# Optimization experiments

Measured on AMD Instinct MI355X. Metric: run time of the kernel, lower is better.

## Reference

```python
import jax, jax.numpy as jnp
import numpy as np
import math

B, T, C, H = 4, 2048, 1024, 16
D = C // H  # head dim = 64


def setup_inputs() -> dict:
    key = jax.random.key(0)
    ks = jax.random.split(key, 5)
    scale = 0.02
    x = jax.random.normal(ks[0], (B, T, C), dtype=jnp.float32)
    # torch nn.Linear(n_embd, 3*n_embd): weight [3C, C]; we store transposed [C, 3C]
    W_kqv = jax.random.normal(ks[1], (C, 3 * C), dtype=jnp.float32) * scale
    b_kqv = jnp.zeros((3 * C,), dtype=jnp.float32)
    W_proj = jax.random.normal(ks[2], (C, C), dtype=jnp.float32) * scale
    b_proj = jnp.zeros((C,), dtype=jnp.float32)
    padding_mask = jnp.ones((B, T), dtype=jnp.int32)  # 1 = valid token
    return {"x": x, "W_kqv": W_kqv, "b_kqv": b_kqv, "W_proj": W_proj,
            "b_proj": b_proj, "padding_mask": padding_mask}


def reference(x, W_kqv, b_kqv, W_proj, b_proj, padding_mask):
    Bx, Tx, Cx = x.shape
    kqv = x @ W_kqv + b_kqv                      # [B,T,3C]
    # original splits as k, q, v (in that order)
    k, q, v = jnp.split(kqv, 3, axis=2)
    def heads(t):
        return t.reshape(Bx, Tx, H, D).transpose(0, 2, 1, 3)  # [B,H,T,D]
    k, q, v = heads(k), heads(q), heads(v)
    att = jnp.einsum('bhqd,bhkd->bhqk', q, k) * (1.0 / math.sqrt(D))  # [B,H,T,T]
    causal = jnp.tril(jnp.ones((Tx, Tx), dtype=bool))[None, None]     # [1,1,T,T]
    valid = causal & (padding_mask[:, None, None, :] != 0)            # [B,1,T,T] broadcast
    neg_inf = jnp.finfo(att.dtype).min
    att = jnp.where(valid, att, neg_inf)
    att = jax.nn.softmax(att, axis=-1)
    y = jnp.einsum('bhqk,bhkd->bhqd', att, v)    # [B,H,T,D]
    y = y.transpose(0, 2, 1, 3).reshape(Bx, Tx, Cx)
    return y @ W_proj + b_proj
```

## Files before the change

### kernel.cpp

```cpp
#include <hip/hip_runtime.h>


typedef short bf16x8 __attribute__((ext_vector_type(8)));
typedef float floatx4 __attribute__((ext_vector_type(4)));

#define MFMA16(a, b, c) __builtin_amdgcn_mfma_f32_16x16x32_bf16(a, b, c, 0, 0, 0)

#define ASYNC_COPY16(gp, lp)                                                   \
  __builtin_amdgcn_global_load_lds(                                            \
      (__attribute__((address_space(1))) void*)(gp),                           \
      (__attribute__((address_space(3))) void*)(lp), 16, 0, 0)

#define DRAIN_VMCNT() asm volatile("s_waitcnt vmcnt(0)" ::: "memory")
#define WAIT_VMCNT6() asm volatile("s_waitcnt vmcnt(6)" ::: "memory")

#if defined(__has_builtin)
#if __has_builtin(__builtin_amdgcn_exp2f)
#define EXP2(x) __builtin_amdgcn_exp2f(x)
#endif
#endif
#ifndef EXP2
#define EXP2(x) exp2f(x)
#endif

__device__ __forceinline__ short f2bf(float f) {
  union { float f; unsigned u; } c;
  c.f = f;
  unsigned r = c.u + 0x7fffu + ((c.u >> 16) & 1u);
  return (short)(r >> 16);
}

__global__ __launch_bounds__(256) void prep(const float* __restrict__ x,
                                            short* __restrict__ xb,
                                            const float* __restrict__ Wkqv,
                                            short* __restrict__ Wkqvt,
                                            const float* __restrict__ Wproj,
                                            short* __restrict__ Wprojt) {
  __shared__ float buf[64][65];
  const int t = threadIdx.x;
  const int bx = blockIdx.x;
  if (bx < 8192) {
    int i = (bx * 256 + t) * 4;
    float4 v = *(const float4*)&x[i];
    short4 o;
    o.x = f2bf(v.x); o.y = f2bf(v.y); o.z = f2bf(v.z); o.w = f2bf(v.w);
    *(short4*)&xb[i] = o;
    return;
  }
  const int tb = bx - 8192;
  const int nb = tb & 63, kb = tb >> 6;
  const float* in;
  short* out;
  int N, n0;
  if (nb < 48) { in = Wkqv; out = Wkqvt; N = 3072; n0 = nb * 64; }
  else         { in = Wproj; out = Wprojt; N = 1024; n0 = (nb - 48) * 64; }
  const int k0 = kb * 64;
#pragma unroll
  for (int i = 0; i < 4; ++i) {
    int s = t + i * 256;
    int row = s >> 4, c4 = (s & 15) * 4;
    float4 v = *(const float4*)&in[(size_t)(k0 + row) * N + n0 + c4];
    buf[row][c4] = v.x; buf[row][c4 + 1] = v.y;
    buf[row][c4 + 2] = v.z; buf[row][c4 + 3] = v.w;
  }
  __syncthreads();
#pragma unroll
  for (int i = 0; i < 2; ++i) {
    int u = t + i * 256;
    int rn = u >> 3, ch = (u & 7) * 8;
    short tmp[8];
#pragma unroll
    for (int j = 0; j < 8; ++j) tmp[j] = f2bf(buf[ch + j][rn]);
    *(uint4*)&out[(size_t)(n0 + rn) * 1024 + k0 + ch] = *(uint4*)tmp;
  }
}

template <int MODE>
__global__ __launch_bounds__(512, 2) void gemm_ph256(const short* __restrict__ A,
                                                     const short* __restrict__ Bt,
                                                     const float* __restrict__ bias,
                                                     void* __restrict__ Cout,
                                                     int M, int N, int K) {
  __shared__ short smem[73728];
  const int tid = threadIdx.x;
  const int lane = tid & 63;
  const int wv = tid >> 6;
  const int l15 = lane & 15, quad = lane >> 4;
  const int xr = l15 & 7;
  int lin = blockIdx.y * gridDim.x + blockIdx.x;
  const int nwg = gridDim.x * gridDim.y;
  lin = (lin & 7) * (nwg >> 3) + (lin >> 3);
  const int bx = lin % gridDim.x, by = lin / gridDim.x;
  const int m0 = by * 128, n0 = bx * 256;
  const int wm = (wv >> 2) * 64, wn = (wv & 3) * 64;
  const int NT = K >> 6;

  floatx4 acc[4][4] = {};

#define STAGE_A(kt, bs, j)                                                     \
  { int c_ = (j) * 512 + tid;                                                  \
    int r_ = c_ >> 3, ch_ = (c_ & 7) ^ (r_ & 7);                               \
    ASYNC_COPY16(&A[(size_t)(m0 + r_) * K + (kt) * 64 + ch_ * 8],              \
                 &smem[(bs) * 8192 + c_ * 8]); }
#define STAGE_B(kt, bs, j)                                                     \
  { int c_ = (j) * 512 + tid;                                                  \
    int r_ = c_ >> 3, ch_ = (c_ & 7) ^ (r_ & 7);                               \
    ASYNC_COPY16(&Bt[(size_t)(n0 + r_) * K + (kt) * 64 + ch_ * 8],             \
                 &smem[24576 + (bs) * 16384 + c_ * 8]); }

  STAGE_A(0, 0, 0); STAGE_A(0, 0, 1);
  STAGE_B(0, 0, 0); STAGE_B(0, 0, 1); STAGE_B(0, 0, 2); STAGE_B(0, 0, 3);
  STAGE_A(1, 1, 0); STAGE_A(1, 1, 1);
  STAGE_B(1, 1, 0); STAGE_B(1, 1, 1); STAGE_B(1, 1, 2); STAGE_B(1, 1, 3);
  WAIT_VMCNT6();
  __builtin_amdgcn_s_barrier();

  int cur = 0, nxt = 2;
  for (int kt = 0; kt < NT; ++kt) {
    const bool st = (kt + 2 < NT);
    const short* Asr = &smem[cur * 8192];
    const short* Bsr = &smem[24576 + cur * 16384];

    if (st) { STAGE_A(kt + 2, nxt, 0); STAGE_A(kt + 2, nxt, 1); STAGE_B(kt + 2, nxt, 0); }
    bf16x8 af[4][2], bf0[2][2];
#pragma unroll
    for (int mi = 0; mi < 4; ++mi)
#pragma unroll
      for (int s = 0; s < 2; ++s)
        af[mi][s] = *(const bf16x8*)
            &Asr[(wm + mi * 16 + l15) * 64 + (((s * 4 + quad) ^ xr) * 8)];
#pragma unroll
    for (int nj = 0; nj < 2; ++nj)
#pragma unroll
      for (int s = 0; s < 2; ++s)
        bf0[nj][s] = *(const bf16x8*)
            &Bsr[(wn + nj * 16 + l15) * 64 + (((s * 4 + quad) ^ xr) * 8)];
    __builtin_amdgcn_s_setprio(1);
#pragma unroll
    for (int s = 0; s < 2; ++s)
#pragma unroll
      for (int mi = 0; mi < 4; ++mi)
#pragma unroll
        for (int nj = 0; nj < 2; ++nj)
          acc[mi][nj] = MFMA16(af[mi][s], bf0[nj][s], acc[mi][nj]);
    __builtin_amdgcn_s_setprio(0);
    __builtin_amdgcn_s_barrier();

    if (st) { STAGE_B(kt + 2, nxt, 1); STAGE_B(kt + 2, nxt, 2); STAGE_B(kt + 2, nxt, 3); }
    bf16x8 bf1[2][2];
#pragma unroll
    for (int nj = 0; nj < 2; ++nj)
#pragma unroll
      for (int s = 0; s < 2; ++s)
        bf1[nj][s] = *(const bf16x8*)
            &Bsr[(wn + (2 + nj) * 16 + l15) * 64 + (((s * 4 + quad) ^ xr) * 8)];
    __builtin_amdgcn_s_setprio(1);
#pragma unroll
    for (int s = 0; s < 2; ++s)
#pragma unroll
      for (int mi = 0; mi < 4; ++mi)
#pragma unroll
        for (int nj = 0; nj < 2; ++nj)
          acc[mi][2 + nj] = MFMA16(af[mi][s], bf1[nj][s], acc[mi][2 + nj]);
    __builtin_amdgcn_s_setprio(0);
    if (st) { WAIT_VMCNT6(); } else { DRAIN_VMCNT(); }
    __builtin_amdgcn_s_barrier();
    cur = (cur == 2) ? 0 : cur + 1;
    nxt = (nxt == 2) ? 0 : nxt + 1;
  }
#undef STAGE_A
#undef STAGE_B

  {
    short* outs = (short*)Cout;
    const size_t QOFF = (size_t)64 * 2048 * 64;
    const int sec = n0 >> 10;
    short* Es = smem;
    if (sec < 2) {
#pragma unroll
      for (int ni = 0; ni < 4; ++ni) {
        int c = wn + ni * 16 + l15;
        float bv = bias[n0 + c];
#pragma unroll
        for (int mi = 0; mi < 4; ++mi) {
          int r0 = wm + mi * 16 + quad * 4;
#pragma unroll
          for (int rr = 0; rr < 4; ++rr) {
            int r = r0 + rr;
            Es[r * 256 + (c ^ (((r >> 2) & 3) << 4))] = f2bf(acc[mi][ni][rr] + bv);
          }
        }
      }
    } else {
#pragma unroll
      for (int ni = 0; ni < 4; ++ni) {
        int c = wn + ni * 16 + l15;
        float bv = bias[n0 + c];
#pragma unroll
        for (int mi = 0; mi < 4; ++mi) {
          int r0 = wm + mi * 16 + quad * 4;
#pragma unroll
          for (int rr = 0; rr < 4; ++rr) {
            int r = r0 + rr;
            Es[c * 128 + (r ^ ((c & 7) << 3))] = f2bf(acc[mi][ni][rr] + bv);
          }
        }
      }
    }
    __syncthreads();
    if (sec < 2) {
#pragma unroll
      for (int jj = 0; jj < 8; ++jj) {
        int idx = jj * 512 + tid;
        int rr2 = idx >> 5;
        int cc2 = (idx & 31) * 8;
        uint4 v = *(const uint4*)&Es[rr2 * 256 + (cc2 ^ (((rr2 >> 2) & 3) << 4))];
        int colg = n0 + cc2;
        int hh = (colg >> 6) & 15, dd = colg & 63;
        int row = m0 + rr2, bb = row >> 11, tt = row & 2047;
        *(uint4*)(outs + (size_t)sec * QOFF +
                  (((size_t)(bb * 16 + hh) * 2048 + tt) * 64 + dd)) = v;
      }
    } else {
#pragma unroll
      for (int jj = 0; jj < 8; ++jj) {
        int idx = jj * 512 + tid;
        int cd = idx >> 4;
        int rb = (idx & 15) * 8;
        uint4 v = *(const uint4*)&Es[cd * 128 + (rb ^ ((cd & 7) << 3))];
        int colg = n0 + cd;
        int hh = (colg >> 6) & 15, dd = colg & 63;
        int trow = m0 + rb, bb = trow >> 11, tt = trow & 2047;
        *(uint4*)(outs + 2 * QOFF +
                  ((size_t)(bb * 16 + hh) * 64 + dd) * 2048 + tt) = v;
      }
    }
  }
}

__global__ __launch_bounds__(256, 2) void gemm_dbuf128(const short* __restrict__ A,
                                                       const short* __restrict__ Bt,
                                                       const float* __restrict__ bias,
                                                       float* __restrict__ outf,
                                                       int M, int N, int K) {
  __shared__ short As[2][8192];
  __shared__ short Bs[2][8192];
  const int tid = threadIdx.x;
  const int lane = tid & 63;
  const int wv = tid >> 6;
  const int l15 = lane & 15, quad = lane >> 4;
  const int xr = l15 & 7;
  int lin = blockIdx.y * gridDim.x + blockIdx.x;
  const int nwg = gridDim.x * gridDim.y;
  lin = (lin & 7) * (nwg >> 3) + (lin >> 3);
  const int bx = lin & (gridDim.x - 1), by = lin / gridDim.x;
  const int m0 = by * 128, n0 = bx * 128;
  const int wm = (wv >> 1) * 64, wn = (wv & 1) * 64;
  const int NT = K >> 6;

  floatx4 acc[4][4] = {};

#define STAGE_AB(kt, bs)                                                       \
  { _Pragma("unroll")                                                          \
    for (int j_ = 0; j_ < 4; ++j_) {                                           \
      int c_ = j_ * 256 + tid;                                                 \
      int r_ = c_ >> 3, ch_ = (c_ & 7) ^ (r_ & 7);                             \
      ASYNC_COPY16(&A[(size_t)(m0 + r_) * K + (kt) * 64 + ch_ * 8],            \
                   &As[bs][c_ * 8]);                                           \
      ASYNC_COPY16(&Bt[(size_t)(n0 + r_) * K + (kt) * 64 + ch_ * 8],           \
                   &Bs[bs][c_ * 8]);                                           \
    } }

  STAGE_AB(0, 0);
  DRAIN_VMCNT();
  __syncthreads();

  int cur = 0;
  for (int kt = 0; kt < NT; ++kt) {
    if (kt + 1 < NT) STAGE_AB(kt + 1, cur ^ 1);
#pragma unroll
    for (int s = 0; s < 2; ++s) {
      const int chs = ((s * 4 + quad) ^ xr) * 8;
      bf16x8 af[4], bfr[4];
#pragma unroll
      for (int i = 0; i < 4; ++i) {
        af[i]  = *(const bf16x8*)&As[cur][(wm + i * 16 + l15) * 64 + chs];
        bfr[i] = *(const bf16x8*)&Bs[cur][(wn + i * 16 + l15) * 64 + chs];
      }
#pragma unroll
      for (int mi = 0; mi < 4; ++mi)
#pragma unroll
        for (int ni = 0; ni < 4; ++ni)
          acc[mi][ni] = MFMA16(af[mi], bfr[ni], acc[mi][ni]);
    }
    DRAIN_VMCNT();
    __syncthreads();
    cur ^= 1;
  }
#undef STAGE_AB

#pragma unroll
  for (int ni = 0; ni < 4; ++ni) {
    int col = n0 + wn + ni * 16 + l15;
    float bv = bias[col];
#pragma unroll
    for (int mi = 0; mi < 4; ++mi) {
#pragma unroll
      for (int rr = 0; rr < 4; ++rr) {
        int row = m0 + wm + mi * 16 + quad * 4 + rr;
        outf[(size_t)row * N + col] = acc[mi][ni][rr] + bv;
      }
    }
  }
}

__global__ __launch_bounds__(256, 3) void attn_flash8(const short* __restrict__ Qd,
                                                      const short* __restrict__ Kd,
                                                      const short* __restrict__ Vd,
                                                      const int* __restrict__ pmask,
                                                      short* __restrict__ y) {
  constexpr int T = 2048, C = 1024;
  __shared__ short Ks[2][64 * 64];
  __shared__ short Vs[2][64 * 64];
  __shared__ short Ps[4][32][64];

  const int tid = threadIdx.x;
  const int lane = tid & 63, w = tid >> 6;
  const int l15 = lane & 15, quad = lane >> 4;
  const int xr = l15 & 7;
  const int lin = blockIdx.x;
  const int qb = 15 - (lin >> 6);
  const int bh = lin & 63;
  const int b = bh >> 4, h = bh & 15;
  const short* Qb = Qd + (size_t)bh * T * 64;
  const short* Kb = Kd + (size_t)bh * T * 64;
  const short* Vb = Vd + (size_t)bh * 64 * T;
  const int* pmi = &pmask[b * T];
  const int q0 = qb * 128;
  const int nt = (q0 >> 6) + 2;

  const float SCALE2 = 0.18033688011112042f;

#define STAGE_KV(t, buf)                                                       \
  {                                                                            \
    const short* ksrc_ = Kb + (size_t)((t) * 64) * 64;                         \
    const short* vsrc_ = Vb + (t) * 64;                                        \
    _Pragma("unroll")                                                          \
    for (int j_ = 0; j_ < 2; ++j_) {                                           \
      int c_ = j_ * 256 + tid;                                                 \
      int r_ = c_ >> 3, cc_ = (c_ & 7) ^ (r_ & 7);                             \
      ASYNC_COPY16(ksrc_ + r_ * 64 + cc_ * 8, &Ks[buf][c_ * 8]);               \
      ASYNC_COPY16(vsrc_ + (size_t)r_ * T + cc_ * 8, &Vs[buf][c_ * 8]);        \
    }                                                                          \
  }

  bf16x8 qf[2][2];
#pragma unroll
  for (int mi = 0; mi < 2; ++mi) {
    const short* qp = Qb + (size_t)(q0 + w * 32 + mi * 16 + l15) * 64;
    qf[mi][0] = *(const bf16x8*)&qp[quad * 8];
    qf[mi][1] = *(const bf16x8*)&qp[32 + quad * 8];
  }

  floatx4 Oacc[2][4] = {};
  float lpart[2] = {};

  STAGE_KV(0, 0);
  DRAIN_VMCNT();
  __syncthreads();

  int cur = 0;
#pragma unroll 1
  for (int t = 0; t < nt; ++t) {
    const int k0 = t * 64;
    if (t + 1 < nt) STAGE_KV(t + 1, cur ^ 1);

    floatx4 Sacc[2][4] = {};
#pragma unroll
    for (int s = 0; s < 2; ++s) {
#pragma unroll
      for (int n4 = 0; n4 < 4; ++n4) {
        bf16x8 bK = *(const bf16x8*)
            &Ks[cur][(n4 * 16 + l15) * 64 + (((s * 4 + quad) ^ xr) * 8)];
        Sacc[0][n4] = MFMA16(bK, qf[0][s], Sacc[0][n4]);
        Sacc[1][n4] = MFMA16(bK, qf[1][s], Sacc[1][n4]);
      }
    }

    if (k0 < q0) {
#pragma unroll
      for (int n4 = 0; n4 < 4; ++n4) {
        int4 pm4 = *(const int4*)&pmi[k0 + n4 * 16 + quad * 4];
        float pb[4];
        pb[0] = pm4.x ? 0.0f : -3.0e38f;
        pb[1] = pm4.y ? 0.0f : -3.0e38f;
        pb[2] = pm4.z ? 0.0f : -3.0e38f;
        pb[3] = pm4.w ? 0.0f : -3.0e38f;
#pragma unroll
        for (int mi = 0; mi < 2; ++mi) {
          float p[4];
#pragma unroll
          for (int rr = 0; rr < 4; ++rr) {
            p[rr] = EXP2(fmaf(Sacc[mi][n4][rr], SCALE2, pb[rr]));
            lpart[mi] += p[rr];
          }
          unsigned lo, hi;
          asm("v_cvt_pk_bf16_f32 %0, %1, %2" : "=v"(lo) : "v"(p[0]), "v"(p[1]));
          asm("v_cvt_pk_bf16_f32 %0, %1, %2" : "=v"(hi) : "v"(p[2]), "v"(p[3]));
          uint2 pk; pk.x = lo; pk.y = hi;
          *(uint2*)&Ps[w][mi * 16 + l15]
                      [((n4 * 2 + (quad >> 1)) ^ xr) * 8 + (quad & 1) * 4] = pk;
        }
      }
    } else {
#pragma unroll
      for (int n4 = 0; n4 < 4; ++n4) {
        int4 pm4 = *(const int4*)&pmi[k0 + n4 * 16 + quad * 4];
        float pb[4];
        pb[0] = pm4.x ? 0.0f : -3.0e38f;
        pb[1] = pm4.y ? 0.0f : -3.0e38f;
        pb[2] = pm4.z ? 0.0f : -3.0e38f;
        pb[3] = pm4.w ? 0.0f : -3.0e38f;
        const int colb = n4 * 16 + quad * 4;
#pragma unroll
        for (int mi = 0; mi < 2; ++mi) {
          const int rowb = (q0 - k0) + w * 32 + mi * 16 + l15;
          float p[4];
#pragma unroll
          for (int rr = 0; rr < 4; ++rr) {
            float v = EXP2(fmaf(Sacc[mi][n4][rr], SCALE2, pb[rr]));
            if (colb + rr > rowb) v = 0.f;
            p[rr] = v;
            lpart[mi] += v;
          }
          unsigned lo, hi;
          asm("v_cvt_pk_bf16_f32 %0, %1, %2" : "=v"(lo) : "v"(p[0]), "v"(p[1]));
          asm("v_cvt_pk_bf16_f32 %0, %1, %2" : "=v"(hi) : "v"(p[2]), "v"(p[3]));
          uint2 pk; pk.x = lo; pk.y = hi;
          *(uint2*)&Ps[w][mi * 16 + l15]
                      [((n4 * 2 + (quad >> 1)) ^ xr) * 8 + (quad & 1) * 4] = pk;
        }
      }
    }

#pragma unroll
    for (int ks2 = 0; ks2 < 2; ++ks2) {
      const int pco = (((ks2 * 4 + quad) ^ xr) * 8);
      bf16x8 ap0 = *(const bf16x8*)&Ps[w][l15][pco];
      bf16x8 ap1 = *(const bf16x8*)&Ps[w][16 + l15][pco];
#pragma unroll
      for (int nd = 0; nd < 4; ++nd) {
        bf16x8 bV = *(const bf16x8*)
            &Vs[cur][(nd * 16 + l15) * 64 + (((ks2 * 4 + quad) ^ xr) * 8)];
        Oacc[0][nd] = MFMA16(ap0, bV, Oacc[0][nd]);
        Oacc[1][nd] = MFMA16(ap1, bV, Oacc[1][nd]);
      }
    }

    DRAIN_VMCNT();
    __syncthreads();
    cur ^= 1;
  }
#undef STAGE_KV

#pragma unroll
  for (int mi = 0; mi < 2; ++mi) {
    float s = lpart[mi];
    s += __shfl_xor(s, 16, 64);
    s += __shfl_xor(s, 32, 64);
    float inv_l[4];
#pragma unroll
    for (int rr = 0; rr < 4; ++rr)
      inv_l[rr] = 1.0f / __shfl(s, quad * 4 + rr, 16);
#pragma unroll
    for (int n = 0; n < 4; ++n) {
      int dcol = n * 16 + l15;
#pragma unroll
      for (int rr = 0; rr < 4; ++rr) {
        int rowq = q0 + w * 32 + mi * 16 + quad * 4 + rr;
        y[((size_t)(b * T + rowq)) * C + h * 64 + dcol] =
            f2bf(Oacc[mi][n][rr] * inv_l[rr]);
      }
    }
  }
}

extern "C" void kernel_launch(void* const* d_in, const int* in_sizes, int n_in,
                              void* d_out, int out_size, void* d_ws, size_t ws_size,
                              hipStream_t stream) {
  constexpr int B = 4, T = 2048, C = 1024;
  constexpr int M = B * T;
  constexpr int N1 = 3 * C;

  const float* x      = (const float*)d_in[0];
  const float* W_kqv  = (const float*)d_in[1];
  const float* b_kqv  = (const float*)d_in[2];
  const float* W_proj = (const float*)d_in[3];
  const float* b_proj = (const float*)d_in[4];
  const int*   pmask  = (const int*)d_in[5];
  float* out = (float*)d_out;

  const size_t QOFF = (size_t)64 * T * 64;

  short* xb     = (short*)d_ws;
  short* Wkqvt  = xb + (size_t)M * C;
  short* Wprojt = Wkqvt + (size_t)N1 * C;
  short* qkv    = Wprojt + (size_t)C * C;
  short* yb     = xb;

  short* Kd = qkv;
  short* Qd = qkv + QOFF;
  short* Vd = qkv + 2 * QOFF;

  prep<<<dim3(8192 + 1024), 256, 0, stream>>>(x, xb, W_kqv, Wkqvt, W_proj, Wprojt);

  gemm_ph256<2><<<dim3(N1 / 256, M / 128), 512, 0, stream>>>(xb, Wkqvt, b_kqv, Kd, M, N1, C);

  attn_flash8<<<dim3(1024), 256, 0, stream>>>(Qd, Kd, Vd, pmask, yb);

  gemm_dbuf128<<<dim3(C / 128, M / 128), 256, 0, stream>>>(yb, Wprojt, b_proj, out, M, C, C);
}
```

Before: 248.1 us.

## Replace QKV GEMM with 256x256 tile, 8-phase double-buffered schedule

The QKV projection GEMM grows from 128x256 tiles with a 3-stage buffer to 256x256 tiles, where each wave computes 128x64. The k-loop processes two 64-wide k-tiles per iteration in an 8-phase schedule that interleaves async loads, LDS reads and MFMA groups with barriers. The goal is more reuse per loaded tile and lower global and LDS traffic per FLOP. In exchange it doubles the accumulator registers, uses only two buffers, adds many barriers, drops the XCD-aware block swizzle, and halves the grid to 384 blocks, which may underfill the CUs.

```diff
diff --git a/kernel.cpp b/kernel.cpp
--- a/kernel.cpp
+++ b/kernel.cpp
@@ -12,7 +12,7 @@
       (__attribute__((address_space(3))) void*)(lp), 16, 0, 0)
 
 #define DRAIN_VMCNT() asm volatile("s_waitcnt vmcnt(0)" ::: "memory")
-#define WAIT_VMCNT6() asm volatile("s_waitcnt vmcnt(6)" ::: "memory")
+#define WAIT_VMCNT(n) asm volatile("s_waitcnt vmcnt(" #n ")" ::: "memory")
 
 #if defined(__has_builtin)
 #if __has_builtin(__builtin_amdgcn_exp2f)
@@ -75,165 +75,173 @@
   }
 }
 
-template <int MODE>
-__global__ __launch_bounds__(512, 2) void gemm_ph256(const short* __restrict__ A,
-                                                     const short* __restrict__ Bt,
-                                                     const float* __restrict__ bias,
-                                                     void* __restrict__ Cout,
-                                                     int M, int N, int K) {
-  __shared__ short smem[73728];
+__global__ __launch_bounds__(512, 2) void gemm_8ph256(const short* __restrict__ A,
+                                                      const short* __restrict__ Bt,
+                                                      const float* __restrict__ bias,
+                                                      short* __restrict__ outs,
+                                                      int M, int N, int K) {
+  __shared__ short smem[65536];
   const int tid = threadIdx.x;
   const int lane = tid & 63;
   const int wv = tid >> 6;
   const int l15 = lane & 15, quad = lane >> 4;
   const int xr = l15 & 7;
-  int lin = blockIdx.y * gridDim.x + blockIdx.x;
-  const int nwg = gridDim.x * gridDim.y;
-  lin = (lin & 7) * (nwg >> 3) + (lin >> 3);
-  const int bx = lin % gridDim.x, by = lin / gridDim.x;
-  const int m0 = by * 128, n0 = bx * 256;
-  const int wm = (wv >> 2) * 64, wn = (wv & 3) * 64;
-  const int NT = K >> 6;
-
-  floatx4 acc[4][4] = {};
-
-#define STAGE_A(kt, bs, j)                                                     \
-  { int c_ = (j) * 512 + tid;                                                  \
-    int r_ = c_ >> 3, ch_ = (c_ & 7) ^ (r_ & 7);                               \
-    ASYNC_COPY16(&A[(size_t)(m0 + r_) * K + (kt) * 64 + ch_ * 8],              \
-                 &smem[(bs) * 8192 + c_ * 8]); }
-#define STAGE_B(kt, bs, j)                                                     \
-  { int c_ = (j) * 512 + tid;                                                  \
-    int r_ = c_ >> 3, ch_ = (c_ & 7) ^ (r_ & 7);                               \
-    ASYNC_COPY16(&Bt[(size_t)(n0 + r_) * K + (kt) * 64 + ch_ * 8],             \
-                 &smem[24576 + (bs) * 16384 + c_ * 8]); }
-
-  STAGE_A(0, 0, 0); STAGE_A(0, 0, 1);
-  STAGE_B(0, 0, 0); STAGE_B(0, 0, 1); STAGE_B(0, 0, 2); STAGE_B(0, 0, 3);
-  STAGE_A(1, 1, 0); STAGE_A(1, 1, 1);
-  STAGE_B(1, 1, 0); STAGE_B(1, 1, 1); STAGE_B(1, 1, 2); STAGE_B(1, 1, 3);
-  WAIT_VMCNT6();
-  __builtin_amdgcn_s_barrier();
-
-  int cur = 0, nxt = 2;
-  for (int kt = 0; kt < NT; ++kt) {
-    const bool st = (kt + 2 < NT);
-    const short* Asr = &smem[cur * 8192];
-    const short* Bsr = &smem[24576 + cur * 16384];
-
-    if (st) { STAGE_A(kt + 2, nxt, 0); STAGE_A(kt + 2, nxt, 1); STAGE_B(kt + 2, nxt, 0); }
-    bf16x8 af[4][2], bf0[2][2];
-#pragma unroll
-    for (int mi = 0; mi < 4; ++mi)
-#pragma unroll
-      for (int s = 0; s < 2; ++s)
-        af[mi][s] = *(const bf16x8*)
-            &Asr[(wm + mi * 16 + l15) * 64 + (((s * 4 + quad) ^ xr) * 8)];
-#pragma unroll
-    for (int nj = 0; nj < 2; ++nj)
-#pragma unroll
-      for (int s = 0; s < 2; ++s)
-        bf0[nj][s] = *(const bf16x8*)
-            &Bsr[(wn + nj * 16 + l15) * 64 + (((s * 4 + quad) ^ xr) * 8)];
-    __builtin_amdgcn_s_setprio(1);
-#pragma unroll
-    for (int s = 0; s < 2; ++s)
-#pragma unroll
-      for (int mi = 0; mi < 4; ++mi)
-#pragma unroll
-        for (int nj = 0; nj < 2; ++nj)
-          acc[mi][nj] = MFMA16(af[mi][s], bf0[nj][s], acc[mi][nj]);
-    __builtin_amdgcn_s_setprio(0);
-    __builtin_amdgcn_s_barrier();
-
-    if (st) { STAGE_B(kt + 2, nxt, 1); STAGE_B(kt + 2, nxt, 2); STAGE_B(kt + 2, nxt, 3); }
-    bf16x8 bf1[2][2];
-#pragma unroll
-    for (int nj = 0; nj < 2; ++nj)
-#pragma unroll
-      for (int s = 0; s < 2; ++s)
-        bf1[nj][s] = *(const bf16x8*)
-            &Bsr[(wn + (2 + nj) * 16 + l15) * 64 + (((s * 4 + quad) ^ xr) * 8)];
-    __builtin_amdgcn_s_setprio(1);
-#pragma unroll
-    for (int s = 0; s < 2; ++s)
-#pragma unroll
-      for (int mi = 0; mi < 4; ++mi)
-#pragma unroll
-        for (int nj = 0; nj < 2; ++nj)
-          acc[mi][2 + nj] = MFMA16(af[mi][s], bf1[nj][s], acc[mi][2 + nj]);
-    __builtin_amdgcn_s_setprio(0);
-    if (st) { WAIT_VMCNT6(); } else { DRAIN_VMCNT(); }
-    __builtin_amdgcn_s_barrier();
-    cur = (cur == 2) ? 0 : cur + 1;
-    nxt = (nxt == 2) ? 0 : nxt + 1;
-  }
-#undef STAGE_A
-#undef STAGE_B
-
-  {
-    short* outs = (short*)Cout;
-    const size_t QOFF = (size_t)64 * 2048 * 64;
-    const int sec = n0 >> 10;
-    short* Es = smem;
-    if (sec < 2) {
-#pragma unroll
-      for (int ni = 0; ni < 4; ++ni) {
-        int c = wn + ni * 16 + l15;
-        float bv = bias[n0 + c];
-#pragma unroll
-        for (int mi = 0; mi < 4; ++mi) {
-          int r0 = wm + mi * 16 + quad * 4;
-#pragma unroll
-          for (int rr = 0; rr < 4; ++rr) {
-            int r = r0 + rr;
-            Es[r * 256 + (c ^ (((r >> 2) & 3) << 4))] = f2bf(acc[mi][ni][rr] + bv);
-          }
+  const int m0 = blockIdx.y * 256, n0 = blockIdx.x * 256;
+  const int wm = (wv >> 2) * 128;
+  const int wn = (wv & 3) * 64;
+  const int NIT = K >> 7;
+
+  const int aoff = (wv >> 2) * 8192;
+  const int boff = 32768 + (wn >> 7) * 8192;
+  const int brow = (wn & 127);
+
+  floatx4 acc[8][4] = {};
+  const int chs0 = (quad ^ xr) * 8, chs1 = ((4 + quad) ^ xr) * 8;
+
+#define STAGE_PA(kt, h)                                                        \
+  { _Pragma("unroll") for (int j_ = 0; j_ < 2; ++j_) {                         \
+      int c_ = j_ * 512 + tid;                                                 \
+      int r_ = c_ >> 3, ch_ = ((c_ & 7) ^ (r_ & 7)) * 8;                       \
+      ASYNC_COPY16(&A[(size_t)(m0 + (h) * 128 + r_) * K + (kt) * 64 + ch_],    \
+                   &smem[((kt) & 1) * 16384 + (h) * 8192 + c_ * 8]); } }
+#define STAGE_PB(kt, h)                                                        \
+  { _Pragma("unroll") for (int j_ = 0; j_ < 2; ++j_) {                         \
+      int c_ = j_ * 512 + tid;                                                 \
+      int r_ = c_ >> 3, ch_ = ((c_ & 7) ^ (r_ & 7)) * 8;                       \
+      ASYNC_COPY16(&Bt[(size_t)(n0 + (h) * 128 + r_) * K + (kt) * 64 + ch_],   \
+                   &smem[32768 + ((kt) & 1) * 16384 + (h) * 8192 + c_ * 8]); } }
+
+#define READ_AF(bo, mb)                                                        \
+  { _Pragma("unroll") for (int i_ = 0; i_ < 4; ++i_) {                         \
+      af[i_][0] = *(const bf16x8*)&smem[aoff + (bo) + ((mb) + i_ * 16 + l15) * 64 + chs0]; \
+      af[i_][1] = *(const bf16x8*)&smem[aoff + (bo) + ((mb) + i_ * 16 + l15) * 64 + chs1]; } }
+#define READ_BF(bo, jb)                                                        \
+  { _Pragma("unroll") for (int j_ = 0; j_ < 2; ++j_) {                         \
+      bf[(jb) + j_][0] = *(const bf16x8*)&smem[boff + (bo) + (brow + ((jb) + j_) * 16 + l15) * 64 + chs0]; \
+      bf[(jb) + j_][1] = *(const bf16x8*)&smem[boff + (bo) + (brow + ((jb) + j_) * 16 + l15) * 64 + chs1]; } }
+#define MMQ(mb, nb)                                                            \
+  { __builtin_amdgcn_s_setprio(1);                                             \
+    _Pragma("unroll") for (int s_ = 0; s_ < 2; ++s_)                           \
+      _Pragma("unroll") for (int i_ = 0; i_ < 4; ++i_)                         \
+        _Pragma("unroll") for (int j_ = 0; j_ < 2; ++j_)                       \
+          acc[(mb) + i_][(nb) + j_] =                                          \
+              MFMA16(af[i_][s_], bf[(nb) + j_][s_], acc[(mb) + i_][(nb) + j_]);\
+    __builtin_amdgcn_s_setprio(0); }
+#define BAR() __builtin_amdgcn_s_barrier()
+
+  STAGE_PA(0, 0); STAGE_PA(0, 1); STAGE_PB(0, 0); STAGE_PB(0, 1);
+
+  for (int it = 0; it < NIT; ++it) {
+    const int t0 = 2 * it;
+    const bool st = (it + 1 < NIT);
+    bf16x8 af[4][2], bf[4][2];
+
+    STAGE_PA(t0 + 1, 0); STAGE_PA(t0 + 1, 1);
+    WAIT_VMCNT(4);
+    BAR();
+    READ_AF(0, 0); READ_BF(0, 0);
+    MMQ(0, 0);
+    BAR();
+    STAGE_PB(t0 + 1, 0); STAGE_PB(t0 + 1, 1);
+    READ_BF(0, 2);
+    BAR();
+    MMQ(0, 2);
+    BAR();
+    READ_AF(0, 64);
+    BAR();
+    MMQ(4, 0);
+    BAR();
+    BAR();
+    MMQ(4, 2);
+    BAR();
+    if (st) { STAGE_PA(t0 + 2, 0); WAIT_VMCNT(2); }
+    else    { DRAIN_VMCNT(); }
+    BAR();
+    READ_AF(16384, 0); READ_BF(16384, 0);
+    MMQ(0, 0);
+    BAR();
+    if (st) { STAGE_PA(t0 + 2, 1); }
+    READ_BF(16384, 2);
+    BAR();
+    MMQ(0, 2);
+    BAR();
+    if (st) { STAGE_PB(t0 + 2, 0); }
+    READ_AF(16384, 64);
+    BAR();
+    MMQ(4, 0);
+    BAR();
+    if (st) { STAGE_PB(t0 + 2, 1); }
+    BAR();
+    MMQ(4, 2);
+    BAR();
+  }
+#undef STAGE_PA
+#undef STAGE_PB
+#undef READ_AF
+#undef READ_BF
+#undef MMQ
+#undef BAR
+
+  const size_t QOFF = (size_t)64 * 2048 * 64;
+  const int sec = n0 >> 10;
+  short* Es = smem;
+  if (sec < 2) {
+#pragma unroll
+    for (int nj = 0; nj < 4; ++nj) {
+      int c = wn + nj * 16 + l15;
+      float bv = bias[n0 + c];
+#pragma unroll
+      for (int mi = 0; mi < 8; ++mi) {
+        int r0 = wm + mi * 16 + quad * 4;
+#pragma unroll
+        for (int rr = 0; rr < 4; ++rr) {
+          int r = r0 + rr;
+          Es[r * 256 + (c ^ (((r >> 2) & 3) << 4))] = f2bf(acc[mi][nj][rr] + bv);
         }
       }
-    } else {
-#pragma unroll
-      for (int ni = 0; ni < 4; ++ni) {
-        int c = wn + ni * 16 + l15;
-        float bv = bias[n0 + c];
-#pragma unroll
-        for (int mi = 0; mi < 4; ++mi) {
-          int r0 = wm + mi * 16 + quad * 4;
-#pragma unroll
-          for (int rr = 0; rr < 4; ++rr) {
-            int r = r0 + rr;
-            Es[c * 128 + (r ^ ((c & 7) << 3))] = f2bf(acc[mi][ni][rr] + bv);
-          }
+    }
+  } else {
+#pragma unroll
+    for (int nj = 0; nj < 4; ++nj) {
+      int c = wn + nj * 16 + l15;
+      float bv = bias[n0 + c];
+#pragma unroll
+      for (int mi = 0; mi < 8; ++mi) {
+        int r0 = wm + mi * 16 + quad * 4;
+#pragma unroll
+        for (int rr = 0; rr < 4; ++rr) {
+          int r = r0 + rr;
+          Es[c * 256 + (r ^ ((c & 7) << 3))] = f2bf(acc[mi][nj][rr] + bv);
         }
       }
     }
-    __syncthreads();
-    if (sec < 2) {
-#pragma unroll
-      for (int jj = 0; jj < 8; ++jj) {
-        int idx = jj * 512 + tid;
-        int rr2 = idx >> 5;
-        int cc2 = (idx & 31) * 8;
-        uint4 v = *(const uint4*)&Es[rr2 * 256 + (cc2 ^ (((rr2 >> 2) & 3) << 4))];
-        int colg = n0 + cc2;
-        int hh = (colg >> 6) & 15, dd = colg & 63;
-        int row = m0 + rr2, bb = row >> 11, tt = row & 2047;
-        *(uint4*)(outs + (size_t)sec * QOFF +
-                  (((size_t)(bb * 16 + hh) * 2048 + tt) * 64 + dd)) = v;
-      }
-    } else {
-#pragma unroll
-      for (int jj = 0; jj < 8; ++jj) {
-        int idx = jj * 512 + tid;
-        int cd = idx >> 4;
-        int rb = (idx & 15) * 8;
-        uint4 v = *(const uint4*)&Es[cd * 128 + (rb ^ ((cd & 7) << 3))];
-        int colg = n0 + cd;
-        int hh = (colg >> 6) & 15, dd = colg & 63;
-        int trow = m0 + rb, bb = trow >> 11, tt = trow & 2047;
-        *(uint4*)(outs + 2 * QOFF +
-                  ((size_t)(bb * 16 + hh) * 64 + dd) * 2048 + tt) = v;
-      }
+  }
+  __syncthreads();
+  if (sec < 2) {
+#pragma unroll
+    for (int jj = 0; jj < 16; ++jj) {
+      int idx = jj * 512 + tid;
+      int rr2 = idx >> 5;
+      int cc2 = (idx & 31) * 8;
+      uint4 v = *(const uint4*)&Es[rr2 * 256 + (cc2 ^ (((rr2 >> 2) & 3) << 4))];
+      int colg = n0 + cc2;
+      int hh = (colg >> 6) & 15, dd = colg & 63;
+      int row = m0 + rr2, bb = row >> 11, tt = row & 2047;
+      *(uint4*)(outs + (size_t)sec * QOFF +
+                (((size_t)(bb * 16 + hh) * 2048 + tt) * 64 + dd)) = v;
+    }
+  } else {
+#pragma unroll
+    for (int jj = 0; jj < 16; ++jj) {
+      int idx = jj * 512 + tid;
+      int cd = idx >> 5;
+      int rb = (idx & 31) * 8;
+      uint4 v = *(const uint4*)&Es[cd * 256 + (rb ^ ((cd & 7) << 3))];
+      int colg = n0 + cd;
+      int hh = (colg >> 6) & 15, dd = colg & 63;
+      int trow = m0 + rb, bb = trow >> 11, tt = trow & 2047;
+      *(uint4*)(outs + 2 * QOFF +
+                ((size_t)(bb * 16 + hh) * 64 + dd) * 2048 + tt) = v;
     }
   }
 }
@@ -514,7 +522,7 @@
 
   prep<<<dim3(8192 + 1024), 256, 0, stream>>>(x, xb, W_kqv, Wkqvt, W_proj, Wprojt);
 
-  gemm_ph256<2><<<dim3(N1 / 256, M / 128), 512, 0, stream>>>(xb, Wkqvt, b_kqv, Kd, M, N1, C);
+  gemm_8ph256<<<dim3(N1 / 256, M / 256), 512, 0, stream>>>(xb, Wkqvt, b_kqv, qkv, M, N1, C);
 
   attn_flash8<<<dim3(1024), 256, 0, stream>>>(Qd, Kd, Vd, pmask, yb);
 
```

Measured after the change: 241.6 us. 1.03x faster.
